# Kernel optimization log

Hardware: AMD Instinct MI355X
Metric: run time of the kernel (lower is better)

Reference implementation:

```python
import jax, jax.numpy as jnp
import numpy as np

B, S, D = 64, 1024, 128
EPS = 1e-5

def hardswish(x):
    return x * jnp.clip(x + 3.0, 0.0, 6.0) / 6.0

def setup_inputs() -> dict:
    key = jax.random.key(0)
    k1, k2, k3 = jax.random.split(key, 3)
    x = jax.random.normal(k1, (B, S, D), dtype=jnp.float32)
    ln_w = jnp.ones((S, D), dtype=jnp.float32)
    ln_b = jnp.zeros((S, D), dtype=jnp.float32)
    # U1[i]/U2[i] rows packed into lower-triangular (S,S); init ~ N(0,1)*0.01
    W1 = jax.random.normal(k2, (S, S), dtype=jnp.float32) * 0.01
    W2 = jax.random.normal(k3, (S, S), dtype=jnp.float32) * 0.01
    return {"x": x, "ln_w": ln_w, "ln_b": ln_b, "W1": W1, "W2": W2}

def reference(x, ln_w, ln_b, W1, W2):
    # LayerNorm over the last two dims (seq_len, feature_dim) jointly
    mu = jnp.mean(x, axis=(-2, -1), keepdims=True)
    var = jnp.mean(jnp.square(x - mu), axis=(-2, -1), keepdims=True)
    h = (x - mu) * jax.lax.rsqrt(var + EPS) * ln_w + ln_b
    # causal (lower-triangular) time mixing: u[:, t] = sum_{s<=t} W1[t, s] * h[:, s]
    mask = jnp.tril(jnp.ones((S, S), dtype=x.dtype))
    u = hardswish(jnp.einsum('ts,bsd->btd', W1 * mask, h))
    v = jnp.einsum('ts,bsd->btd', W2 * mask, u)
    return x + v
```

## Files before the change

### kernel.cpp

```cpp
#include <hip/hip_runtime.h>
#include <hip/hip_bf16.h>

#define NB 64
#define S_ 1024
#define D_ 128

typedef __attribute__((ext_vector_type(8))) short bf16x8;
typedef __attribute__((ext_vector_type(4))) float f32x4;
typedef __attribute__((ext_vector_type(4))) unsigned int u32x4;


__device__ __forceinline__ unsigned short f2bf(float f) {
  __hip_bfloat16 h = __float2bfloat16(f);
  return __builtin_bit_cast(unsigned short, h);
}

__device__ __forceinline__ void async_copy16(const void* g, void* l) {
  __builtin_amdgcn_global_load_lds(
      (const __attribute__((address_space(1))) unsigned int*)g,
      (__attribute__((address_space(3))) unsigned int*)l, 16, 0, 0);
}

__device__ __forceinline__ void store16_dev(void* p, bf16x8 v) {
  u32x4 d = __builtin_bit_cast(u32x4, v);
  asm volatile("global_store_dwordx4 %0, %1, off sc1" ::"v"(p), "v"(d)
               : "memory");
}

__device__ __forceinline__ void spin_mask(unsigned* p, unsigned need) {
  if (threadIdx.x == 0) {
    int guard = 0;
    while ((__hip_atomic_load(p, __ATOMIC_RELAXED, __HIP_MEMORY_SCOPE_AGENT) &
            need) != need) {
      __builtin_amdgcn_s_sleep(1);
      if (++guard > 2000000) break;
    }
  }
  __syncthreads();
  asm volatile("" ::: "memory");
}

__device__ __forceinline__ void publish_bit(unsigned* p, unsigned bit) {
  asm volatile("s_waitcnt vmcnt(0)" ::: "memory");
  __syncthreads();
  if (threadIdx.x == 0)
    __hip_atomic_fetch_or(p, bit, __ATOMIC_RELAXED, __HIP_MEMORY_SCOPE_AGENT);
}

__global__ __launch_bounds__(256) void wpack_kernel(
    const float* __restrict__ W1, const float* __restrict__ W2,
    unsigned short* __restrict__ W1f, unsigned short* __restrict__ W2f,
    unsigned* __restrict__ stats) {
  const int blk = blockIdx.x;
  const int t = threadIdx.x;
  const int wave = t >> 6, lane = t & 63;
  const int quad = lane >> 4, l16 = lane & 15;
  if (blk == 0) {
#pragma unroll
    for (int i = 0; i < 8; ++i) stats[t + i * 256] = 0u;
  }
#pragma unroll
  for (int rep = 0; rep < 2; ++rep) {
    const int u = blk * 8 + wave * 2 + rep;
    const int f = u & 2047;
    const int p = f >> 5, c = f & 31;
    const int r = p * 16 + l16;
    const int k0 = c * 32 + quad * 8;
    const float* wsrc = ((u >> 11) ? W2 : W1) + (size_t)r * 1024 + k0;
    float4 a0 = ((const float4*)wsrc)[0];
    float4 a1 = ((const float4*)wsrc)[1];
    float av[8] = {a0.x, a0.y, a0.z, a0.w, a1.x, a1.y, a1.z, a1.w};
    bf16x8 o;
#pragma unroll
    for (int jj = 0; jj < 8; ++jj)
      o[jj] = (short)f2bf((k0 + jj <= r) ? av[jj] : 0.f);
    unsigned short* dstp = ((u >> 11) ? W2f : W1f) +
                           ((size_t)p * 32 + c) * 512 + lane * 8;
    *(bf16x8*)dstp = o;
  }
}

template <bool HSWISH>
__device__ __forceinline__ void gemm_phase(
    unsigned short* ldsA, const int b, const int mt, unsigned* flags,
    const unsigned short* __restrict__ Af, const unsigned short* __restrict__ Bf,
    unsigned short* __restrict__ Uf, const float* __restrict__ Xres,
    float* __restrict__ Out) {
  const int t = threadIdx.x;
  const int wave = t >> 6, lane = t & 63;
  const int quad = lane >> 4, l16 = lane & 15;
  const int row0 = mt * 64;

  const int cend = 2 * (mt + 1);
  const int npan = (cend + 7) >> 3;

  const unsigned short* Ab = Af + (size_t)mt * 4 * 32 * 512;
  const unsigned short* Bb = Bf + (size_t)b * (D_ * S_);

  {
    const int C = (cend - 1 < 11) ? (cend - 1) : 11;
    spin_mask(flags, (2u << (C >> 1)) - 1u);
  }

  f32x4 acc[4][2] = {};
  bf16x8 Bp[4][2];
#pragma unroll
  for (int g = 0; g < 4; ++g) {
    const int gg = (g < cend) ? g : 0;
#pragma unroll
    for (int jj = 0; jj < 2; ++jj)
      Bp[g][jj] = *(const bf16x8*)(Bb + ((size_t)(wave * 2 + jj) * 32 + gg) * 512 + lane * 8);
  }

  for (int p = 0; p < npan; ++p) {
    if (p) {
      const int C = (cend - 1 < p * 8 + 11) ? (cend - 1) : (p * 8 + 11);
      spin_mask(flags, (2u << (C >> 1)) - 1u);
    }
    const int rem = cend - p * 8;
#pragma unroll
    for (int jc = 0; jc < 8; ++jc) {
      const int flat16 = jc * 256 + t;
      const int iw = flat16 >> 9;
      const int cc = (flat16 >> 6) & 7;
      const int li = flat16 & 63;
      if (cc < rem)
        async_copy16(Ab + ((size_t)iw * 32 + p * 8 + cc) * 512 + li * 8,
                     ldsA + flat16 * 8);
    }
    __syncthreads();
#pragma unroll
    for (int c = 0; c < 8; ++c) {
      const int g = p * 8 + c;
      if (g < cend) {
        bf16x8 af[4];
#pragma unroll
        for (int i = 0; i < 4; ++i)
          af[i] = *(const bf16x8*)(ldsA + i * 4096 + c * 512 + lane * 8);
        __builtin_amdgcn_s_setprio(1);
#pragma unroll
        for (int i = 0; i < 4; ++i)
#pragma unroll
          for (int jj = 0; jj < 2; ++jj)
            acc[i][jj] = __builtin_amdgcn_mfma_f32_16x16x32_bf16(
                af[i], Bp[c & 3][jj], acc[i][jj], 0, 0, 0);
        __builtin_amdgcn_s_setprio(0);
        const int gn = (g + 4 < cend) ? (g + 4) : 0;
#pragma unroll
        for (int jj = 0; jj < 2; ++jj)
          Bp[c & 3][jj] = *(const bf16x8*)(
              Bb + ((size_t)(wave * 2 + jj) * 32 + gn) * 512 + lane * 8);
      }
    }
  }

  if (HSWISH) {
    __syncthreads();
    unsigned short* ldsT = ldsA;
#pragma unroll
    for (int i = 0; i < 4; ++i)
#pragma unroll
      for (int jj = 0; jj < 2; ++jj) {
        ushort4 pk;
        float v0 = acc[i][jj][0], v1 = acc[i][jj][1], v2 = acc[i][jj][2], v3 = acc[i][jj][3];
        pk.x = f2bf(v0 * fminf(fmaxf(v0 + 3.f, 0.f), 6.f) * (1.f / 6.f));
        pk.y = f2bf(v1 * fminf(fmaxf(v1 + 3.f, 0.f), 6.f) * (1.f / 6.f));
        pk.z = f2bf(v2 * fminf(fmaxf(v2 + 3.f, 0.f), 6.f) * (1.f / 6.f));
        pk.w = f2bf(v3 * fminf(fmaxf(v3 + 3.f, 0.f), 6.f) * (1.f / 6.f));
        const int n = wave * 32 + jj * 16 + l16;
        const int m0 = i * 16 + quad * 4;
        *(ushort4*)(ldsT + n * 72 + m0) = pk;
      }
    __syncthreads();
    unsigned short* gU = Uf + (size_t)b * (D_ * S_);
#pragma unroll
    for (int ff = 0; ff < 4; ++ff) {
      const int f = wave * 4 + ff;
      const int p2 = f >> 1, cl = f & 1;
      const int d = p2 * 16 + l16;
      const int tb = cl * 32 + quad * 8;
      bf16x8 v = *(const bf16x8*)(ldsT + d * 72 + tb);
      store16_dev(gU + ((size_t)p2 * 32 + mt * 2 + cl) * 512 + lane * 8, v);
    }
  } else {
    float* gO = Out + (size_t)b * S_ * D_;
    const float* gX = Xres + (size_t)b * S_ * D_;
#pragma unroll
    for (int i = 0; i < 4; ++i) {
      const int mrow0 = row0 + i * 16 + quad * 4;
#pragma unroll
      for (int jj = 0; jj < 2; ++jj) {
        const int col = wave * 32 + jj * 16 + l16;
#pragma unroll
        for (int r = 0; r < 4; ++r) {
          const int addr = (mrow0 + r) * D_ + col;
          gO[addr] = gX[addr] + acc[i][jj][r];
        }
      }
    }
  }
}

__global__ __launch_bounds__(256, 4) void mega_kernel(
    const float* __restrict__ x, const float* __restrict__ ln_w,
    const float* __restrict__ ln_b, const unsigned short* __restrict__ W1f,
    const unsigned short* __restrict__ W2f, float* __restrict__ stats,
    unsigned short* __restrict__ hTf, unsigned short* __restrict__ uTf,
    float* __restrict__ out) {
  __shared__ __align__(16) unsigned short smem[16384];

  const int bi = blockIdx.x;
  const int xcd = bi & 7;
  const int slot = bi >> 3;
  const int b = xcd * 8 + (slot & 7);
  const int j = slot >> 3;
  const int mt = (j < 8) ? j : (j ^ 3);

  const int t = threadIdx.x;
  const int wave = t >> 6, lane = t & 63;
  const int quad = lane >> 4, l16 = lane & 15;

  float* sb = stats + (size_t)b * 32;
  unsigned* cntp = (unsigned*)sb + 2;
  unsigned* hmp = (unsigned*)sb + 4;
  unsigned* ump = (unsigned*)sb + 6;

  float2* w4 = (float2*)(smem + 8448);
  float* mr = (float*)(smem + 8464);

  const float4* xb = (const float4*)(x + ((size_t)b * S_ + mt * 64) * D_);
  {
    float s = 0.f, q = 0.f;
#pragma unroll
    for (int i = 0; i < 8; ++i) {
      float4 v = xb[i * 256 + t];
      s += v.x + v.y + v.z + v.w;
      q += v.x * v.x + v.y * v.y + v.z * v.z + v.w * v.w;
    }
#pragma unroll
    for (int o = 32; o > 0; o >>= 1) {
      s += __shfl_down(s, o, 64);
      q += __shfl_down(q, o, 64);
    }
    if (lane == 0) w4[wave] = make_float2(s, q);
  }
  __syncthreads();
  if (t == 0) {
    float ss = 0.f, qq = 0.f;
#pragma unroll
    for (int i = 0; i < 4; ++i) { ss += w4[i].x; qq += w4[i].y; }
    float o1 = __hip_atomic_fetch_add(sb + 0, ss, __ATOMIC_RELAXED,
                                      __HIP_MEMORY_SCOPE_AGENT);
    float o2 = __hip_atomic_fetch_add(sb + 1, qq, __ATOMIC_RELAXED,
                                      __HIP_MEMORY_SCOPE_AGENT);
    asm volatile("" ::"v"(o1), "v"(o2));
    __hip_atomic_fetch_add(cntp, 1u, __ATOMIC_RELAXED,
                           __HIP_MEMORY_SCOPE_AGENT);
    int guard = 0;
    while (__hip_atomic_load(cntp, __ATOMIC_RELAXED,
                             __HIP_MEMORY_SCOPE_AGENT) < 16u) {
      __builtin_amdgcn_s_sleep(1);
      if (++guard > 2000000) break;
    }
    float s1 = __hip_atomic_load(sb + 0, __ATOMIC_RELAXED,
                                 __HIP_MEMORY_SCOPE_AGENT);
    float s2 = __hip_atomic_load(sb + 1, __ATOMIC_RELAXED,
                                 __HIP_MEMORY_SCOPE_AGENT);
    const float inv = 1.0f / (S_ * D_);
    const float mu = s1 * inv;
    mr[0] = mu;
    mr[1] = rsqrtf(s2 * inv - mu * mu + 1e-5f);
  }
  __syncthreads();
  const float mu = mr[0];
  const float rs = mr[1];

  {
    unsigned short* lds = smem;
    const float4* wb = (const float4*)(ln_w + (size_t)(mt * 64) * D_);
    const float4* bv4 = (const float4*)(ln_b + (size_t)(mt * 64) * D_);
#pragma unroll
    for (int r = 0; r < 8; ++r) {
      const int f = r * 256 + t;
      const int srow = f >> 5;
      const int c4 = f & 31;
      float4 xv = xb[f];
      float4 wv = wb[f];
      float4 bvv = bv4[f];
      ushort4 o;
      o.x = f2bf((xv.x - mu) * rs * wv.x + bvv.x);
      o.y = f2bf((xv.y - mu) * rs * wv.y + bvv.y);
      o.z = f2bf((xv.z - mu) * rs * wv.z + bvv.z);
      o.w = f2bf((xv.w - mu) * rs * wv.w + bvv.w);
      *(ushort4*)(lds + srow * 132 + c4 * 4) = o;
    }
    __syncthreads();
    unsigned short* outp = hTf + (size_t)b * (D_ * S_);
    const int cg0 = mt * 2;
#pragma unroll
    for (int ff = 0; ff < 4; ++ff) {
      const int f = wave * 4 + ff;
      const int p = f >> 1, cl = f & 1;
      const int d = p * 16 + l16;
      const int sbase = cl * 32 + quad * 8;
      bf16x8 v;
#pragma unroll
      for (int jj = 0; jj < 8; ++jj)
        v[jj] = (short)lds[(sbase + jj) * 132 + d];
      store16_dev(outp + ((size_t)p * 32 + cg0 + cl) * 512 + lane * 8, v);
    }
  }
  publish_bit(hmp, 1u << mt);

  gemm_phase<true>(smem, b, mt, hmp, W1f, hTf, uTf, nullptr, nullptr);
  publish_bit(ump, 1u << mt);

  gemm_phase<false>(smem, b, mt, ump, W2f, uTf, nullptr, x, out);
}

extern "C" void kernel_launch(void* const* d_in, const int* in_sizes, int n_in,
                              void* d_out, int out_size, void* d_ws, size_t ws_size,
                              hipStream_t stream) {
  const float* x = (const float*)d_in[0];
  const float* ln_w = (const float*)d_in[1];
  const float* ln_b = (const float*)d_in[2];
  const float* W1 = (const float*)d_in[3];
  const float* W2 = (const float*)d_in[4];
  float* out = (float*)d_out;

  char* ws = (char*)d_ws;
  float* stats = (float*)ws;
  unsigned short* W1f = (unsigned short*)(ws + 16384);
  unsigned short* W2f = W1f + (size_t)S_ * S_;
  unsigned short* hTf = W2f + (size_t)S_ * S_;
  unsigned short* uTf = hTf + (size_t)NB * D_ * S_;

  wpack_kernel<<<512, 256, 0, stream>>>(W1, W2, W1f, W2f, (unsigned*)stats);
  mega_kernel<<<1024, 256, 0, stream>>>(x, ln_w, ln_b, W1f, W2f, stats,
                                        hTf, uTf, out);
}
```

Baseline: 133.9 us.

## Double-buffer A-panel LDS staging with explicit vmcnt waits in causal GEMM

Replaces the single 8-chunk LDS panel load followed by __syncthreads with a two-stage double buffer of 4-chunk quarters. Asynchronous global-to-LDS copies for the next quarter are issued while MFMAs consume the current one, synchronized by hand-counted s_waitcnt vmcnt values and raw barriers. The flag spin-wait also changes from per-panel progressive waits to a single upfront wait on all needed row tiles. This aims to hide load latency, at the cost of fragile vmcnt accounting and possibly more time spent waiting on flags at the start.

```diff
diff --git a/kernel.cpp b/kernel.cpp
--- a/kernel.cpp
+++ b/kernel.cpp
@@ -92,15 +92,29 @@
   const int row0 = mt * 64;
 
   const int cend = 2 * (mt + 1);
-  const int npan = (cend + 7) >> 3;
+  const int nq = (cend + 3) >> 2;
 
   const unsigned short* Ab = Af + (size_t)mt * 4 * 32 * 512;
   const unsigned short* Bb = Bf + (size_t)b * (D_ * S_);
 
-  {
-    const int C = (cend - 1 < 11) ? (cend - 1) : 11;
-    spin_mask(flags, (2u << (C >> 1)) - 1u);
-  }
+  spin_mask(flags, (2u << mt) - 1);
+
+  auto STAGE = [&](int q) {
+    unsigned short* buf = ldsA + (q & 1) * 8192;
+    const int c0 = q * 4;
+    if (wave < cend - c0) {
+#pragma unroll
+      for (int jc = 0; jc < 4; ++jc) {
+        const int flat16 = jc * 256 + t;
+        async_copy16(Ab + ((size_t)jc * 32 + c0 + wave) * 512 + lane * 8,
+                     buf + flat16 * 8);
+      }
+    }
+  };
+
+  STAGE(0);
+  if (nq > 1) STAGE(1);
+  __builtin_amdgcn_sched_barrier(0);
 
   f32x4 acc[4][2] = {};
   bf16x8 Bp[4][2];
@@ -112,46 +126,41 @@
       Bp[g][jj] = *(const bf16x8*)(Bb + ((size_t)(wave * 2 + jj) * 32 + gg) * 512 + lane * 8);
   }
 
-  for (int p = 0; p < npan; ++p) {
-    if (p) {
-      const int C = (cend - 1 < p * 8 + 11) ? (cend - 1) : (p * 8 + 11);
-      spin_mask(flags, (2u << (C >> 1)) - 1u);
-    }
-    const int rem = cend - p * 8;
-#pragma unroll
-    for (int jc = 0; jc < 8; ++jc) {
-      const int flat16 = jc * 256 + t;
-      const int iw = flat16 >> 9;
-      const int cc = (flat16 >> 6) & 7;
-      const int li = flat16 & 63;
-      if (cc < rem)
-        async_copy16(Ab + ((size_t)iw * 32 + p * 8 + cc) * 512 + li * 8,
-                     ldsA + flat16 * 8);
-    }
-    __syncthreads();
-#pragma unroll
-    for (int c = 0; c < 8; ++c) {
-      const int g = p * 8 + c;
+  for (int q = 0; q < nq; ++q) {
+    if (q < nq - 1)
+      asm volatile("s_waitcnt vmcnt(12)" ::: "memory");
+    else
+      asm volatile("s_waitcnt vmcnt(8)" ::: "memory");
+    __builtin_amdgcn_s_barrier();
+    __builtin_amdgcn_sched_barrier(0);
+    unsigned short* buf = ldsA + (q & 1) * 8192;
+#pragma unroll
+    for (int c = 0; c < 4; ++c) {
+      const int g = q * 4 + c;
       if (g < cend) {
         bf16x8 af[4];
 #pragma unroll
         for (int i = 0; i < 4; ++i)
-          af[i] = *(const bf16x8*)(ldsA + i * 4096 + c * 512 + lane * 8);
+          af[i] = *(const bf16x8*)(buf + i * 2048 + c * 512 + lane * 8);
         __builtin_amdgcn_s_setprio(1);
 #pragma unroll
         for (int i = 0; i < 4; ++i)
 #pragma unroll
           for (int jj = 0; jj < 2; ++jj)
             acc[i][jj] = __builtin_amdgcn_mfma_f32_16x16x32_bf16(
-                af[i], Bp[c & 3][jj], acc[i][jj], 0, 0, 0);
+                af[i], Bp[c][jj], acc[i][jj], 0, 0, 0);
         __builtin_amdgcn_s_setprio(0);
-        const int gn = (g + 4 < cend) ? (g + 4) : 0;
-#pragma unroll
-        for (int jj = 0; jj < 2; ++jj)
-          Bp[c & 3][jj] = *(const bf16x8*)(
-              Bb + ((size_t)(wave * 2 + jj) * 32 + gn) * 512 + lane * 8);
       }
-    }
+      const int gn = (g + 4 < cend) ? (g + 4) : 0;
+#pragma unroll
+      for (int jj = 0; jj < 2; ++jj)
+        Bp[c][jj] = *(const bf16x8*)(
+            Bb + ((size_t)(wave * 2 + jj) * 32 + gn) * 512 + lane * 8);
+    }
+    __builtin_amdgcn_sched_barrier(0);
+    __builtin_amdgcn_s_barrier();
+    __builtin_amdgcn_sched_barrier(0);
+    if (q + 2 < nq) STAGE(q + 2);
   }
 
   if (HSWISH) {
```

New measurement: 131.2 us. 1.02x faster.

## Move LayerNorm stats to prep kernel and split GEMM phases across blocks

Applied to the files above, without the earlier changes.

The per-batch LayerNorm statistics are now computed in the pre-pack kernel, which removes the in-kernel spin barrier on a block counter. The mega kernel launches twice as many blocks: the first group does the LayerNorm and the first GEMM and publishes flags, and the second group does the second GEMM, waiting on those flags. LDS per block is halved by staging A in 4-chunk panels and transposing the hardswish output in two halves, so occupancy bounds can rise to 8 blocks per CU. This adds a memset launch and depends on all blocks being co-resident, since the second-group blocks spin on flags set by first-group blocks.

```diff
diff --git a/kernel.cpp b/kernel.cpp
--- a/kernel.cpp
+++ b/kernel.cpp
@@ -47,17 +47,43 @@
     __hip_atomic_fetch_or(p, bit, __ATOMIC_RELAXED, __HIP_MEMORY_SCOPE_AGENT);
 }
 
-__global__ __launch_bounds__(256) void wpack_kernel(
-    const float* __restrict__ W1, const float* __restrict__ W2,
-    unsigned short* __restrict__ W1f, unsigned short* __restrict__ W2f,
-    unsigned* __restrict__ stats) {
+__global__ __launch_bounds__(256) void prep_kernel(
+    const float* __restrict__ x, const float* __restrict__ W1,
+    const float* __restrict__ W2, float* __restrict__ stats,
+    unsigned short* __restrict__ W1f, unsigned short* __restrict__ W2f) {
+  __shared__ float2 w4[4];
   const int blk = blockIdx.x;
   const int t = threadIdx.x;
   const int wave = t >> 6, lane = t & 63;
   const int quad = lane >> 4, l16 = lane & 15;
-  if (blk == 0) {
-#pragma unroll
-    for (int i = 0; i < 8; ++i) stats[t + i * 256] = 0u;
+
+  if (blk < 256) {
+    const int b = blk >> 2, sl = blk & 3;
+    const float4* xb =
+        (const float4*)(x + (size_t)b * (S_ * D_) + (size_t)sl * (256 * D_));
+    float s = 0.f, q = 0.f;
+#pragma unroll
+    for (int i = 0; i < 32; ++i) {
+      float4 v = xb[i * 256 + t];
+      s += v.x + v.y + v.z + v.w;
+      q += v.x * v.x + v.y * v.y + v.z * v.z + v.w * v.w;
+    }
+#pragma unroll
+    for (int o = 32; o > 0; o >>= 1) {
+      s += __shfl_down(s, o, 64);
+      q += __shfl_down(q, o, 64);
+    }
+    if (lane == 0) w4[wave] = make_float2(s, q);
+    __syncthreads();
+    if (t == 0) {
+      float ss = 0.f, qq = 0.f;
+#pragma unroll
+      for (int i = 0; i < 4; ++i) { ss += w4[i].x; qq += w4[i].y; }
+      __hip_atomic_fetch_add(stats + (size_t)b * 32 + 0, ss, __ATOMIC_RELAXED,
+                             __HIP_MEMORY_SCOPE_AGENT);
+      __hip_atomic_fetch_add(stats + (size_t)b * 32 + 1, qq, __ATOMIC_RELAXED,
+                             __HIP_MEMORY_SCOPE_AGENT);
+    }
   }
 #pragma unroll
   for (int rep = 0; rep < 2; ++rep) {
@@ -92,13 +118,13 @@
   const int row0 = mt * 64;
 
   const int cend = 2 * (mt + 1);
-  const int npan = (cend + 7) >> 3;
+  const int nhp = (cend + 3) >> 2;
 
   const unsigned short* Ab = Af + (size_t)mt * 4 * 32 * 512;
   const unsigned short* Bb = Bf + (size_t)b * (D_ * S_);
 
   {
-    const int C = (cend - 1 < 11) ? (cend - 1) : 11;
+    const int C = (cend - 1 < 7) ? (cend - 1) : 7;
     spin_mask(flags, (2u << (C >> 1)) - 1u);
   }
 
@@ -112,75 +138,79 @@
       Bp[g][jj] = *(const bf16x8*)(Bb + ((size_t)(wave * 2 + jj) * 32 + gg) * 512 + lane * 8);
   }
 
-  for (int p = 0; p < npan; ++p) {
-    if (p) {
-      const int C = (cend - 1 < p * 8 + 11) ? (cend - 1) : (p * 8 + 11);
+  for (int hp = 0; hp < nhp; ++hp) {
+    if (hp) {
+      const int C = (cend - 1 < hp * 4 + 7) ? (cend - 1) : (hp * 4 + 7);
       spin_mask(flags, (2u << (C >> 1)) - 1u);
     }
-    const int rem = cend - p * 8;
-#pragma unroll
-    for (int jc = 0; jc < 8; ++jc) {
-      const int flat16 = jc * 256 + t;
-      const int iw = flat16 >> 9;
-      const int cc = (flat16 >> 6) & 7;
-      const int li = flat16 & 63;
-      if (cc < rem)
-        async_copy16(Ab + ((size_t)iw * 32 + p * 8 + cc) * 512 + li * 8,
-                     ldsA + flat16 * 8);
+    const int rem = cend - hp * 4;
+    if (wave < rem) {
+#pragma unroll
+      for (int jc = 0; jc < 4; ++jc)
+        async_copy16(Ab + ((size_t)jc * 32 + hp * 4 + wave) * 512 + lane * 8,
+                     ldsA + ((size_t)jc * 256 + t) * 8);
     }
     __syncthreads();
 #pragma unroll
-    for (int c = 0; c < 8; ++c) {
-      const int g = p * 8 + c;
+    for (int c = 0; c < 4; ++c) {
+      const int g = hp * 4 + c;
       if (g < cend) {
         bf16x8 af[4];
 #pragma unroll
         for (int i = 0; i < 4; ++i)
-          af[i] = *(const bf16x8*)(ldsA + i * 4096 + c * 512 + lane * 8);
+          af[i] = *(const bf16x8*)(ldsA + i * 2048 + c * 512 + lane * 8);
         __builtin_amdgcn_s_setprio(1);
 #pragma unroll
         for (int i = 0; i < 4; ++i)
 #pragma unroll
           for (int jj = 0; jj < 2; ++jj)
             acc[i][jj] = __builtin_amdgcn_mfma_f32_16x16x32_bf16(
-                af[i], Bp[c & 3][jj], acc[i][jj], 0, 0, 0);
+                af[i], Bp[c][jj], acc[i][jj], 0, 0, 0);
         __builtin_amdgcn_s_setprio(0);
-        const int gn = (g + 4 < cend) ? (g + 4) : 0;
-#pragma unroll
-        for (int jj = 0; jj < 2; ++jj)
-          Bp[c & 3][jj] = *(const bf16x8*)(
-              Bb + ((size_t)(wave * 2 + jj) * 32 + gn) * 512 + lane * 8);
-      }
+      }
+      const int gn = (g + 4 < cend) ? (g + 4) : 0;
+#pragma unroll
+      for (int jj = 0; jj < 2; ++jj)
+        Bp[c][jj] = *(const bf16x8*)(
+            Bb + ((size_t)(wave * 2 + jj) * 32 + gn) * 512 + lane * 8);
     }
   }
 
   if (HSWISH) {
-    __syncthreads();
-    unsigned short* ldsT = ldsA;
-#pragma unroll
-    for (int i = 0; i < 4; ++i)
-#pragma unroll
-      for (int jj = 0; jj < 2; ++jj) {
-        ushort4 pk;
-        float v0 = acc[i][jj][0], v1 = acc[i][jj][1], v2 = acc[i][jj][2], v3 = acc[i][jj][3];
-        pk.x = f2bf(v0 * fminf(fmaxf(v0 + 3.f, 0.f), 6.f) * (1.f / 6.f));
-        pk.y = f2bf(v1 * fminf(fmaxf(v1 + 3.f, 0.f), 6.f) * (1.f / 6.f));
-        pk.z = f2bf(v2 * fminf(fmaxf(v2 + 3.f, 0.f), 6.f) * (1.f / 6.f));
-        pk.w = f2bf(v3 * fminf(fmaxf(v3 + 3.f, 0.f), 6.f) * (1.f / 6.f));
-        const int n = wave * 32 + jj * 16 + l16;
-        const int m0 = i * 16 + quad * 4;
-        *(ushort4*)(ldsT + n * 72 + m0) = pk;
-      }
-    __syncthreads();
-    unsigned short* gU = Uf + (size_t)b * (D_ * S_);
-#pragma unroll
-    for (int ff = 0; ff < 4; ++ff) {
-      const int f = wave * 4 + ff;
-      const int p2 = f >> 1, cl = f & 1;
-      const int d = p2 * 16 + l16;
-      const int tb = cl * 32 + quad * 8;
-      bf16x8 v = *(const bf16x8*)(ldsT + d * 72 + tb);
-      store16_dev(gU + ((size_t)p2 * 32 + mt * 2 + cl) * 512 + lane * 8, v);
+    unsigned short* scr = ldsA;
+#pragma unroll
+    for (int half = 0; half < 2; ++half) {
+      __syncthreads();
+      if ((wave >> 1) == half) {
+#pragma unroll
+        for (int i = 0; i < 4; ++i)
+#pragma unroll
+          for (int jj = 0; jj < 2; ++jj) {
+            ushort4 pk;
+            float v0 = acc[i][jj][0], v1 = acc[i][jj][1], v2 = acc[i][jj][2],
+                  v3 = acc[i][jj][3];
+            pk.x = f2bf(v0 * fminf(fmaxf(v0 + 3.f, 0.f), 6.f) * (1.f / 6.f));
+            pk.y = f2bf(v1 * fminf(fmaxf(v1 + 3.f, 0.f), 6.f) * (1.f / 6.f));
+            pk.z = f2bf(v2 * fminf(fmaxf(v2 + 3.f, 0.f), 6.f) * (1.f / 6.f));
+            pk.w = f2bf(v3 * fminf(fmaxf(v3 + 3.f, 0.f), 6.f) * (1.f / 6.f));
+            const int nl = (wave & 1) * 32 + jj * 16 + l16;
+            const int m0 = i * 16 + quad * 4;
+            *(ushort4*)(scr + nl * 72 + m0) = pk;
+          }
+      }
+      __syncthreads();
+      unsigned short* gU = Uf + (size_t)b * (D_ * S_);
+#pragma unroll
+      for (int ff = 0; ff < 2; ++ff) {
+        const int f = wave * 2 + ff;
+        const int p2l = f >> 1, cl = f & 1;
+        const int dl = p2l * 16 + l16;
+        const int tb = cl * 32 + quad * 8;
+        bf16x8 v = *(const bf16x8*)(scr + dl * 72 + tb);
+        store16_dev(gU + ((size_t)(half * 4 + p2l) * 32 + mt * 2 + cl) * 512 +
+                        lane * 8,
+                    v);
+      }
     }
   } else {
     float* gO = Out + (size_t)b * S_ * D_;
@@ -201,17 +231,19 @@
   }
 }
 
-__global__ __launch_bounds__(256, 4) void mega_kernel(
+__global__ __launch_bounds__(256, 8) void mega_kernel(
     const float* __restrict__ x, const float* __restrict__ ln_w,
     const float* __restrict__ ln_b, const unsigned short* __restrict__ W1f,
     const unsigned short* __restrict__ W2f, float* __restrict__ stats,
     unsigned short* __restrict__ hTf, unsigned short* __restrict__ uTf,
     float* __restrict__ out) {
-  __shared__ __align__(16) unsigned short smem[16384];
+  __shared__ __align__(16) unsigned short smem[8480];
 
   const int bi = blockIdx.x;
-  const int xcd = bi & 7;
-  const int slot = bi >> 3;
+  const int grp = bi >> 10;
+  const int inner = bi & 1023;
+  const int xcd = inner & 7;
+  const int slot = inner >> 3;
   const int b = xcd * 8 + (slot & 7);
   const int j = slot >> 3;
   const int mt = (j < 8) ? j : (j ^ 3);
@@ -221,101 +253,57 @@
   const int quad = lane >> 4, l16 = lane & 15;
 
   float* sb = stats + (size_t)b * 32;
-  unsigned* cntp = (unsigned*)sb + 2;
   unsigned* hmp = (unsigned*)sb + 4;
   unsigned* ump = (unsigned*)sb + 6;
 
-  float2* w4 = (float2*)(smem + 8448);
-  float* mr = (float*)(smem + 8464);
-
-  const float4* xb = (const float4*)(x + ((size_t)b * S_ + mt * 64) * D_);
-  {
-    float s = 0.f, q = 0.f;
-#pragma unroll
-    for (int i = 0; i < 8; ++i) {
-      float4 v = xb[i * 256 + t];
-      s += v.x + v.y + v.z + v.w;
-      q += v.x * v.x + v.y * v.y + v.z * v.z + v.w * v.w;
-    }
-#pragma unroll
-    for (int o = 32; o > 0; o >>= 1) {
-      s += __shfl_down(s, o, 64);
-      q += __shfl_down(q, o, 64);
-    }
-    if (lane == 0) w4[wave] = make_float2(s, q);
-  }
-  __syncthreads();
-  if (t == 0) {
-    float ss = 0.f, qq = 0.f;
-#pragma unroll
-    for (int i = 0; i < 4; ++i) { ss += w4[i].x; qq += w4[i].y; }
-    float o1 = __hip_atomic_fetch_add(sb + 0, ss, __ATOMIC_RELAXED,
-                                      __HIP_MEMORY_SCOPE_AGENT);
-    float o2 = __hip_atomic_fetch_add(sb + 1, qq, __ATOMIC_RELAXED,
-                                      __HIP_MEMORY_SCOPE_AGENT);
-    asm volatile("" ::"v"(o1), "v"(o2));
-    __hip_atomic_fetch_add(cntp, 1u, __ATOMIC_RELAXED,
-                           __HIP_MEMORY_SCOPE_AGENT);
-    int guard = 0;
-    while (__hip_atomic_load(cntp, __ATOMIC_RELAXED,
-                             __HIP_MEMORY_SCOPE_AGENT) < 16u) {
-      __builtin_amdgcn_s_sleep(1);
-      if (++guard > 2000000) break;
-    }
-    float s1 = __hip_atomic_load(sb + 0, __ATOMIC_RELAXED,
-                                 __HIP_MEMORY_SCOPE_AGENT);
-    float s2 = __hip_atomic_load(sb + 1, __ATOMIC_RELAXED,
-                                 __HIP_MEMORY_SCOPE_AGENT);
+  if (grp == 0) {
     const float inv = 1.0f / (S_ * D_);
-    const float mu = s1 * inv;
-    mr[0] = mu;
-    mr[1] = rsqrtf(s2 * inv - mu * mu + 1e-5f);
-  }
-  __syncthreads();
-  const float mu = mr[0];
-  const float rs = mr[1];
-
-  {
-    unsigned short* lds = smem;
-    const float4* wb = (const float4*)(ln_w + (size_t)(mt * 64) * D_);
-    const float4* bv4 = (const float4*)(ln_b + (size_t)(mt * 64) * D_);
-#pragma unroll
-    for (int r = 0; r < 8; ++r) {
-      const int f = r * 256 + t;
-      const int srow = f >> 5;
-      const int c4 = f & 31;
-      float4 xv = xb[f];
-      float4 wv = wb[f];
-      float4 bvv = bv4[f];
-      ushort4 o;
-      o.x = f2bf((xv.x - mu) * rs * wv.x + bvv.x);
-      o.y = f2bf((xv.y - mu) * rs * wv.y + bvv.y);
-      o.z = f2bf((xv.z - mu) * rs * wv.z + bvv.z);
-      o.w = f2bf((xv.w - mu) * rs * wv.w + bvv.w);
-      *(ushort4*)(lds + srow * 132 + c4 * 4) = o;
-    }
-    __syncthreads();
-    unsigned short* outp = hTf + (size_t)b * (D_ * S_);
-    const int cg0 = mt * 2;
-#pragma unroll
-    for (int ff = 0; ff < 4; ++ff) {
-      const int f = wave * 4 + ff;
-      const int p = f >> 1, cl = f & 1;
-      const int d = p * 16 + l16;
-      const int sbase = cl * 32 + quad * 8;
-      bf16x8 v;
-#pragma unroll
-      for (int jj = 0; jj < 8; ++jj)
-        v[jj] = (short)lds[(sbase + jj) * 132 + d];
-      store16_dev(outp + ((size_t)p * 32 + cg0 + cl) * 512 + lane * 8, v);
-    }
-  }
-  publish_bit(hmp, 1u << mt);
-
-  gemm_phase<true>(smem, b, mt, hmp, W1f, hTf, uTf, nullptr, nullptr);
-  publish_bit(ump, 1u << mt);
-
-  gemm_phase<false>(smem, b, mt, ump, W2f, uTf, nullptr, x, out);
+    const float mu = sb[0] * inv;
+    const float rs = rsqrtf(sb[1] * inv - mu * mu + 1e-5f);
+
+    {
+      unsigned short* lds = smem;
+      const float4* xb = (const float4*)(x + ((size_t)b * S_ + mt * 64) * D_);
+      const float4* wb = (const float4*)(ln_w + (size_t)(mt * 64) * D_);
+      const float4* bv4 = (const float4*)(ln_b + (size_t)(mt * 64) * D_);
+#pragma unroll
+      for (int rr = 0; rr < 8; ++rr) {
+        const int f = rr * 256 + t;
+        const int srow = f >> 5;
+        const int c4 = f & 31;
+        float4 xv = xb[f];
+        float4 wv = wb[f];
+        float4 bvv = bv4[f];
+        ushort4 o;
+        o.x = f2bf((xv.x - mu) * rs * wv.x + bvv.x);
+        o.y = f2bf((xv.y - mu) * rs * wv.y + bvv.y);
+        o.z = f2bf((xv.z - mu) * rs * wv.z + bvv.z);
+        o.w = f2bf((xv.w - mu) * rs * wv.w + bvv.w);
+        *(ushort4*)(lds + srow * 132 + c4 * 4) = o;
+      }
+      __syncthreads();
+      unsigned short* outp = hTf + (size_t)b * (D_ * S_);
+      const int cg0 = mt * 2;
+#pragma unroll
+      for (int ff = 0; ff < 4; ++ff) {
+        const int f = wave * 4 + ff;
+        const int p = f >> 1, cl = f & 1;
+        const int d = p * 16 + l16;
+        const int sbase = cl * 32 + quad * 8;
+        bf16x8 v;
+#pragma unroll
+        for (int jj = 0; jj < 8; ++jj)
+          v[jj] = (short)lds[(sbase + jj) * 132 + d];
+        store16_dev(outp + ((size_t)p * 32 + cg0 + cl) * 512 + lane * 8, v);
+      }
+    }
+    publish_bit(hmp, 1u << mt);
+
+    gemm_phase<true>(smem, b, mt, hmp, W1f, hTf, uTf, nullptr, nullptr);
+    publish_bit(ump, 1u << mt);
+  } else {
+    gemm_phase<false>(smem, b, mt, ump, W2f, uTf, nullptr, x, out);
+  }
 }
 
 extern "C" void kernel_launch(void* const* d_in, const int* in_sizes, int n_in,
@@ -335,7 +323,8 @@
   unsigned short* hTf = W2f + (size_t)S_ * S_;
   unsigned short* uTf = hTf + (size_t)NB * D_ * S_;
 
-  wpack_kernel<<<512, 256, 0, stream>>>(W1, W2, W1f, W2f, (unsigned*)stats);
-  mega_kernel<<<1024, 256, 0, stream>>>(x, ln_w, ln_b, W1f, W2f, stats,
+  hipMemsetAsync(stats, 0, 8192, stream);
+  prep_kernel<<<512, 256, 0, stream>>>(x, W1, W2, stats, W1f, W2f);
+  mega_kernel<<<2048, 256, 0, stream>>>(x, ln_w, ln_b, W1f, W2f, stats,
                                         hTf, uTf, out);
 }
```

Result: slower. 360.6 us (+169.3%).
